# Kernel tuning notes

Hardware: AMD Instinct MI355X
Metric: run time of the kernel (lower is better)

The kernel has to match this reference:

```python
import jax, jax.numpy as jnp
import numpy as np

B, S, D, H, FF, L = 2, 2048, 512, 8, 2048, 2
HD = D // H
EPS = 1e-5
NEG = -1e9


def layernorm(x, gamma, beta):
    # mean/var over last axis (axis=2 in original)
    mean = jnp.mean(x, axis=-1, keepdims=True)
    var = jnp.mean((x - mean) ** 2, axis=-1, keepdims=True)
    return gamma * (x - mean) / jnp.sqrt(var + EPS) + beta


def masked_attention(x, mask, Wqkv, Wo, bo):
    b, s, d = x.shape
    qkv = x @ Wqkv                                  # [B,S,3D]
    qkv = qkv.reshape(b, s, H, 3 * HD)
    qkv = qkv.reshape(b, H, s, 3 * HD)              # original uses reshape, not transpose
    q, k, v = jnp.split(qkv, 3, axis=3)             # each [B,H,S,HD]
    scaled = jnp.einsum('bhqd,bhkd->bhqk', q, k) / (HD ** 0.5)
    col = mask[:, None, None, :]                    # valid key columns
    row = mask[:, None, :, None]                    # valid query rows
    logits = jnp.where(col, scaled, NEG)
    attn = jax.nn.softmax(logits, axis=-1)
    attn = attn * (row & col).astype(attn.dtype)    # exact zeros outside valid block
    values = jnp.einsum('bhqk,bhkd->bhqd', attn, v)  # [B,H,S,HD]
    values = values.reshape(b, s, H * HD)           # original uses reshape, not transpose
    return values @ Wo + bo


def encoder_layer(x, mask, p):
    res = x
    x = masked_attention(x, mask, p['Wqkv'], p['Wo'], p['bo'])
    x = layernorm(x + res, p['g1'], p['be1'])
    res = x
    x = jax.nn.relu(x @ p['W1'] + p['bf1']) @ p['W2'] + p['bf2']
    x = layernorm(x + res, p['g2'], p['be2'])
    return x


def setup_inputs() -> dict:
    key = jax.random.key(0)
    ks = jax.random.split(key, 8)
    x = jax.random.normal(ks[0], (B, S, D), jnp.float32)
    lengths = jax.random.randint(ks[1], (B,), S // 2, S + 1)
    paded_mask = jnp.arange(S)[None, :] < lengths[:, None]   # [B,S] bool
    sc = 0.02
    return {
        'x': x,
        'paded_mask': paded_mask,
        'Wqkv': jax.random.normal(ks[2], (L, D, 3 * D), jnp.float32) * sc,
        'Wo': jax.random.normal(ks[3], (L, D, D), jnp.float32) * sc,
        'bo': jnp.zeros((L, D), jnp.float32),
        'g1': jnp.ones((L, D), jnp.float32),
        'be1': jnp.zeros((L, D), jnp.float32),
        'W1': jax.random.normal(ks[4], (L, D, FF), jnp.float32) * sc,
        'bf1': jnp.zeros((L, FF), jnp.float32),
        'W2': jax.random.normal(ks[5], (L, FF, D), jnp.float32) * sc,
        'bf2': jnp.zeros((L, D), jnp.float32),
        'g2': jnp.ones((L, D), jnp.float32),
        'be2': jnp.zeros((L, D), jnp.float32),
    }


def reference(x, paded_mask, Wqkv, Wo, bo, g1, be1, W1, bf1, W2, bf2, g2, be2):
    for i in range(L):
        p = {'Wqkv': Wqkv[i], 'Wo': Wo[i], 'bo': bo[i], 'g1': g1[i], 'be1': be1[i],
             'W1': W1[i], 'bf1': bf1[i], 'W2': W2[i], 'bf2': bf2[i], 'g2': g2[i], 'be2': be2[i]}
        x = encoder_layer(x, paded_mask, p)
    return x
```

## Files before the change

### kernel.cpp

```cpp
#include <hip/hip_runtime.h>
#include <math.h>


typedef __bf16 bf16x8 __attribute__((ext_vector_type(8)));
typedef __bf16 bf16x4 __attribute__((ext_vector_type(4)));
typedef float f32x4 __attribute__((ext_vector_type(4)));

static constexpr int S_ = 2048;
static constexpr int D_ = 512;
static constexpr int FF_ = 2048;
static constexpr int M_ = 4096;

#define GLDS16(gp, lp)                                                      \
  __builtin_amdgcn_global_load_lds(                                         \
      (const __attribute__((address_space(1))) void*)(gp),                  \
      (__attribute__((address_space(3))) void*)(lp), 16, 0, 0)

__global__ __launch_bounds__(256) void prep_kernel(
    const float* __restrict__ Wqkv, const float* __restrict__ Wo,
    const float* __restrict__ W1, const float* __restrict__ W2,
    const float* __restrict__ x,
    __bf16* __restrict__ WqkvT, __bf16* __restrict__ WoT,
    __bf16* __restrict__ W1T, __bf16* __restrict__ W2T,
    __bf16* __restrict__ x_bf) {
  __shared__ float tile[32][33];
  const int t = threadIdx.x;
  int bid = blockIdx.x;
  if (bid >= 6144) {
    const size_t i = ((size_t)(bid - 6144) * 256 + t) * 8;
    float4 f0 = *(const float4*)(x + i), f1 = *(const float4*)(x + i + 4);
    bf16x8 v;
    v[0] = (__bf16)f0.x; v[1] = (__bf16)f0.y; v[2] = (__bf16)f0.z; v[3] = (__bf16)f0.w;
    v[4] = (__bf16)f1.x; v[5] = (__bf16)f1.y; v[6] = (__bf16)f1.z; v[7] = (__bf16)f1.w;
    *(bf16x8*)(x_bf + i) = v;
    return;
  }
  const float* W;
  __bf16* Wt;
  int K, N;
  if (bid < 1536)      { W = Wqkv;              Wt = WqkvT; K = 512;  N = 1536; }
  else if (bid < 2048) { bid -= 1536; W = Wo;   Wt = WoT;   K = 512;  N = 512; }
  else if (bid < 4096) { bid -= 2048; W = W1;   Wt = W1T;   K = 512;  N = 2048; }
  else                 { bid -= 4096; W = W2;   Wt = W2T;   K = 2048; N = 512; }
  const int nx = N >> 5, ny = K >> 5;
  const int xb = bid % nx, yb = (bid / nx) % ny, l = bid / (nx * ny);
  const size_t off = (size_t)l * K * N;
  const int n0 = xb * 32, k0 = yb * 32;
  const int tx = t & 31, ty = t >> 5;
#pragma unroll
  for (int i = 0; i < 4; ++i)
    tile[ty + i * 8][tx] = W[off + (size_t)(k0 + ty + i * 8) * N + n0 + tx];
  __syncthreads();
#pragma unroll
  for (int i = 0; i < 4; ++i)
    Wt[off + (size_t)(n0 + ty + i * 8) * K + k0 + tx] = (__bf16)tile[tx][ty + i * 8];
}

template <int BN, bool RELU, bool SPLITK2, bool QKV, bool OUT_BF16>
__global__ __launch_bounds__(256) void gemm_async(
    const __bf16* __restrict__ A, const __bf16* __restrict__ Wt,
    const float* __restrict__ bias, void* __restrict__ Cv,
    __bf16* __restrict__ VT, int M, int N, int K) {
  constexpr int BM = 128, BK = 64;
  constexpr int MI = 4;
  constexpr int NJ = BN / 32;
  __shared__ __bf16 As[BM][BK];
  __shared__ __bf16 Bs[BN][BK];

  const int t = threadIdx.x;
  const int wv = t >> 6, ln = t & 63;
  const int ln16 = t & 15, quad = (t & 63) >> 4;
  const int bm = blockIdx.x * BM, bn = blockIdx.y * BN;
  const int wm = (wv & 1) * 64, wn = (wv >> 1) * (BN / 2);

  int kbeg = 0, kend = K;
  if (SPLITK2) {
    const int half = K >> 1;
    kbeg = blockIdx.z * half;
    kend = kbeg + half;
  }

  f32x4 acc[MI][NJ];
#pragma unroll
  for (int i = 0; i < MI; ++i)
#pragma unroll
    for (int j = 0; j < NJ; ++j) acc[i][j] = {0.f, 0.f, 0.f, 0.f};

  for (int k0 = kbeg; k0 < kend; k0 += BK) {
#pragma unroll
    for (int it = 0; it < 4; ++it) {
      const int cb = it * 256 + wv * 64;
      const int c = cb + ln;
      const int r = c >> 3, jl = (c & 7) ^ (r & 7);
      GLDS16(A + (size_t)(bm + r) * K + k0 + jl * 8,
             (char*)&As[0][0] + (size_t)cb * 16);
    }
#pragma unroll
    for (int it = 0; it < BN / 32; ++it) {
      const int cb = it * 256 + wv * 64;
      const int c = cb + ln;
      const int r = c >> 3, jl = (c & 7) ^ (r & 7);
      GLDS16(Wt + (size_t)(bn + r) * K + k0 + jl * 8,
             (char*)&Bs[0][0] + (size_t)cb * 16);
    }
    __syncthreads();

#pragma unroll
    for (int kk = 0; kk < 2; ++kk) {
      bf16x8 a[MI], b[NJ];
#pragma unroll
      for (int i = 0; i < MI; ++i) {
        const int r = wm + i * 16 + ln16;
        a[i] = *(const bf16x8*)&As[r][((kk * 4 + quad) ^ (r & 7)) * 8];
      }
#pragma unroll
      for (int j = 0; j < NJ; ++j) {
        const int r = wn + j * 16 + ln16;
        b[j] = *(const bf16x8*)&Bs[r][((kk * 4 + quad) ^ (r & 7)) * 8];
      }
#pragma unroll
      for (int i = 0; i < MI; ++i)
#pragma unroll
        for (int j = 0; j < NJ; ++j)
          acc[i][j] = __builtin_amdgcn_mfma_f32_16x16x32_bf16(a[i], b[j], acc[i][j], 0, 0, 0);
    }
    __syncthreads();
  }

  float* Cs = (float*)Cv;
  if (SPLITK2) Cs += (size_t)blockIdx.z * M * N;
  const bool addb = bias && (!SPLITK2 || blockIdx.z == 0);
  const int bidx = bm >> 11;
#pragma unroll
  for (int i = 0; i < MI; ++i) {
#pragma unroll
    for (int j = 0; j < NJ; ++j) {
      const int col = bn + wn + j * 16 + ln16;
      if (QKV && (col % 192) >= 128) {
        const int d = col % 192 - 128;
        const int n8 = col / 192;
#pragma unroll
        for (int r = 0; r < 4; ++r) {
          const int s = (bm + wm + i * 16 + quad * 4 + r) & 2047;
          const int h = s >> 8;
          const int s2 = ((s & 255) << 3) | n8;
          VT[(((size_t)(bidx * 8 + h) * 64 + d) << 11) + s2] = (__bf16)acc[i][j][r];
        }
      } else {
        const float bv = addb ? bias[col] : 0.f;
#pragma unroll
        for (int r = 0; r < 4; ++r) {
          const int row = bm + wm + i * 16 + quad * 4 + r;
          float v = acc[i][j][r] + bv;
          if (RELU) v = fmaxf(v, 0.f);
          if (OUT_BF16)
            ((__bf16*)Cv)[(size_t)row * N + col] = (__bf16)v;
          else
            Cs[(size_t)row * N + col] = v;
        }
      }
    }
  }
}

__global__ __launch_bounds__(256) void attn_mfma(
    const __bf16* __restrict__ qkv, const __bf16* __restrict__ VT,
    const int* __restrict__ mask, __bf16* __restrict__ O) {
  const int b = blockIdx.z;
  const int h = blockIdx.y;
  const int q0 = blockIdx.x * 64;
  const int t = threadIdx.x;
  const int wq = t >> 6, ln16 = t & 15, quad = (t & 63) >> 4;

  __shared__ __bf16 Ks[64][72];
  __shared__ __bf16 Vt[64][72];
  __shared__ __bf16 Ps[64][72];
  __shared__ int lred[4];
  __shared__ int len_sh;

  const __bf16* base = qkv + (size_t)b * S_ * 1536 + (size_t)h * S_ * 192;
  const __bf16* vbase = VT + ((size_t)(b * 8 + h) << 17);
  __bf16* obase = O + (size_t)b * S_ * 512 + h * 64;

  {
    int c = 0;
    const int* mp = mask + b * S_ + t * 8;
#pragma unroll
    for (int i = 0; i < 8; ++i) c += mp[i];
#pragma unroll
    for (int off = 32; off >= 1; off >>= 1) c += __shfl_down(c, off, 64);
    if ((t & 63) == 0) lred[t >> 6] = c;
  }
  __syncthreads();
  if (t == 0) len_sh = lred[0] + lred[1] + lred[2] + lred[3];
  __syncthreads();
  const int len = len_sh;

  if (q0 >= len) {
    const int r = t >> 2, c16 = (t & 3) * 16;
    bf16x8 z = {};
    *(bf16x8*)(obase + (size_t)(q0 + r) * 512 + c16) = z;
    *(bf16x8*)(obase + (size_t)(q0 + r) * 512 + c16 + 8) = z;
    return;
  }

  bf16x8 aq[2];
  {
    const int q = q0 + wq * 16 + ln16;
    aq[0] = *(const bf16x8*)(base + (size_t)q * 192 + quad * 8);
    aq[1] = *(const bf16x8*)(base + (size_t)q * 192 + 32 + quad * 8);
  }

  float lpart = 0.f;
  f32x4 o[4];
#pragma unroll
  for (int d = 0; d < 4; ++d) o[d] = {0.f, 0.f, 0.f, 0.f};

  const int kr = t >> 3, kc = (t & 7) * 8;
  const int vd = t >> 2, vc = (t & 3) * 16;
  const int vphys = vc ^ ((vd & 3) * 16);

  bf16x8 kreg[2], vreg[2];
  auto fetch = [&](int kt) {
    kreg[0] = *(const bf16x8*)(base + (size_t)(kt + kr) * 192 + 64 + kc);
    kreg[1] = *(const bf16x8*)(base + (size_t)(kt + kr + 32) * 192 + 64 + kc);
    const __bf16* vp = vbase + (size_t)vd * 2048 + kt + vc;
    vreg[0] = *(const bf16x8*)vp;
    vreg[1] = *(const bf16x8*)(vp + 8);
  };

  fetch(0);

  for (int k0 = 0; k0 < len; k0 += 64) {
    *(bf16x8*)&Ks[kr][kc] = kreg[0];
    *(bf16x8*)&Ks[kr + 32][kc] = kreg[1];
    *(bf16x8*)&Vt[vd][vphys] = vreg[0];
    *(bf16x8*)&Vt[vd][vphys + 8] = vreg[1];
    __syncthreads();

    { const int kp = (k0 + 64 < S_) ? k0 + 64 : k0; fetch(kp); }

    f32x4 sf[4];
#pragma unroll
    for (int j = 0; j < 4; ++j) sf[j] = {0.f, 0.f, 0.f, 0.f};
#pragma unroll
    for (int kk = 0; kk < 2; ++kk) {
#pragma unroll
      for (int j = 0; j < 4; ++j) {
        bf16x8 ak = *(const bf16x8*)&Ks[j * 16 + ln16][kk * 32 + quad * 8];
        sf[j] = __builtin_amdgcn_mfma_f32_16x16x32_bf16(ak, aq[kk], sf[j], 0, 0, 0);
      }
    }

#pragma unroll
    for (int j = 0; j < 4; ++j) {
      bf16x4 pk;
#pragma unroll
      for (int r = 0; r < 4; ++r) {
        const float e = __expf(fminf(sf[j][r] * 0.125f, 60.f));
        const float p = (k0 + j * 16 + quad * 4 + r < len) ? e : 0.f;
        lpart += p;
        pk[r] = (__bf16)p;
      }
      *(bf16x4*)&Ps[wq * 16 + ln16][j * 16 + quad * 4] = pk;
    }
    asm volatile("s_waitcnt lgkmcnt(0)" ::: "memory");

#pragma unroll
    for (int kk = 0; kk < 2; ++kk) {
      bf16x8 pb = *(const bf16x8*)&Ps[wq * 16 + ln16][kk * 32 + quad * 8];
#pragma unroll
      for (int dt = 0; dt < 4; ++dt) {
        bf16x8 av = *(const bf16x8*)
            &Vt[dt * 16 + ln16][(kk * 32 + quad * 8) ^ ((ln16 & 3) * 16)];
        o[dt] = __builtin_amdgcn_mfma_f32_16x16x32_bf16(av, pb, o[dt], 0, 0, 0);
      }
    }
    __syncthreads();
  }

  lpart += __shfl_xor(lpart, 16, 64);
  lpart += __shfl_xor(lpart, 32, 64);

  const int q = q0 + wq * 16 + ln16;
  const float s = (q < len) ? 1.f / lpart : 0.f;
#pragma unroll
  for (int dt = 0; dt < 4; ++dt) {
    bf16x4 ov;
#pragma unroll
    for (int r = 0; r < 4; ++r) ov[r] = (__bf16)(o[dt][r] * s);
    *(bf16x4*)(obase + (size_t)q * 512 + dt * 16 + quad * 4) = ov;
  }
}

__global__ __launch_bounds__(256) void add_ln_kernel(
    const float* __restrict__ a, const float* __restrict__ a2,
    const float* __restrict__ res, const float* __restrict__ g,
    const float* __restrict__ be, float* __restrict__ out,
    __bf16* __restrict__ out_bf) {
  const int row = blockIdx.x * 4 + (threadIdx.x >> 6);
  const int ln = threadIdx.x & 63;
  const int c = ln * 8;
  const float* pa = a + (size_t)row * D_ + c;
  const float* pr = res + (size_t)row * D_ + c;

  float4 v0 = *(const float4*)pa, v1 = *(const float4*)(pa + 4);
  float4 r0 = *(const float4*)pr, r1 = *(const float4*)(pr + 4);
  float w[8] = {v0.x + r0.x, v0.y + r0.y, v0.z + r0.z, v0.w + r0.w,
                v1.x + r1.x, v1.y + r1.y, v1.z + r1.z, v1.w + r1.w};
  if (a2) {
    const float* p2 = a2 + (size_t)row * D_ + c;
    float4 u0 = *(const float4*)p2, u1 = *(const float4*)(p2 + 4);
    w[0] += u0.x; w[1] += u0.y; w[2] += u0.z; w[3] += u0.w;
    w[4] += u1.x; w[5] += u1.y; w[6] += u1.z; w[7] += u1.w;
  }
  float s = 0.f, sq = 0.f;
#pragma unroll
  for (int e = 0; e < 8; ++e) {
    s += w[e];
    sq += w[e] * w[e];
  }
#pragma unroll
  for (int off = 1; off < 64; off <<= 1) {
    s += __shfl_xor(s, off, 64);
    sq += __shfl_xor(sq, off, 64);
  }
  const float mean = s * (1.0f / D_);
  const float var = sq * (1.0f / D_) - mean * mean;
  const float rstd = rsqrtf(var + 1e-5f);

  float4 g0 = *(const float4*)(g + c), g1 = *(const float4*)(g + c + 4);
  float4 b0 = *(const float4*)(be + c), b1 = *(const float4*)(be + c + 4);
  const float gv[8] = {g0.x, g0.y, g0.z, g0.w, g1.x, g1.y, g1.z, g1.w};
  const float bv[8] = {b0.x, b0.y, b0.z, b0.w, b1.x, b1.y, b1.z, b1.w};
  float y[8];
#pragma unroll
  for (int e = 0; e < 8; ++e) y[e] = gv[e] * (w[e] - mean) * rstd + bv[e];

  float* po = out + (size_t)row * D_ + c;
  *(float4*)po = make_float4(y[0], y[1], y[2], y[3]);
  *(float4*)(po + 4) = make_float4(y[4], y[5], y[6], y[7]);
  if (out_bf) {
    bf16x8 v;
#pragma unroll
    for (int e = 0; e < 8; ++e) v[e] = (__bf16)y[e];
    *(bf16x8*)(out_bf + (size_t)row * D_ + c) = v;
  }
}

extern "C" void kernel_launch(void* const* d_in, const int* in_sizes, int n_in,
                              void* d_out, int out_size, void* d_ws, size_t ws_size,
                              hipStream_t stream) {
  const float* x_in = (const float*)d_in[0];
  const int* mask   = (const int*)d_in[1];
  const float* Wqkv = (const float*)d_in[2];
  const float* Wo   = (const float*)d_in[3];
  const float* bo   = (const float*)d_in[4];
  const float* g1   = (const float*)d_in[5];
  const float* be1  = (const float*)d_in[6];
  const float* W1   = (const float*)d_in[7];
  const float* bf1  = (const float*)d_in[8];
  const float* W2   = (const float*)d_in[9];
  const float* bf2  = (const float*)d_in[10];
  const float* g2   = (const float*)d_in[11];
  const float* be2  = (const float*)d_in[12];
  float* out = (float*)d_out;

  char* w = (char*)d_ws;
  auto alloc = [&](size_t bytes) {
    char* p = w;
    w += (bytes + 255) & ~(size_t)255;
    return p;
  };
  __bf16* WqkvT = (__bf16*)alloc((size_t)2 * 512 * 1536 * 2);
  __bf16* WoT   = (__bf16*)alloc((size_t)2 * 512 * 512 * 2);
  __bf16* W1T   = (__bf16*)alloc((size_t)2 * 512 * 2048 * 2);
  __bf16* W2T   = (__bf16*)alloc((size_t)2 * 2048 * 512 * 2);
  __bf16* R1    = (__bf16*)alloc((size_t)M_ * FF_ * 2);
  __bf16* VTb   = (__bf16*)alloc((size_t)16 * 64 * 2048 * 2);
  float* R2     = (float*)alloc((size_t)2 * M_ * D_ * 4);
  __bf16* Obf   = (__bf16*)alloc((size_t)M_ * D_ * 2);
  float* proj   = (float*)alloc((size_t)M_ * D_ * 4);
  float* x1     = (float*)alloc((size_t)M_ * D_ * 4);
  float* xE     = (float*)alloc((size_t)M_ * D_ * 4);
  __bf16* x_bf  = (__bf16*)alloc((size_t)M_ * D_ * 2);
  __bf16* x1_bf = (__bf16*)alloc((size_t)M_ * D_ * 2);
  __bf16* xE_bf = (__bf16*)alloc((size_t)M_ * D_ * 2);

  prep_kernel<<<dim3(7168), 256, 0, stream>>>(Wqkv, Wo, W1, W2, x_in,
                                              WqkvT, WoT, W1T, W2T, x_bf);

  for (int l = 0; l < 2; ++l) {
    const float* xin = (l == 0) ? x_in : xE;
    const __bf16* xin_bf = (l == 0) ? x_bf : xE_bf;
    float* xout = (l == 1) ? out : xE;
    __bf16* xout_bf = (l == 0) ? xE_bf : nullptr;
    const __bf16* WqkvT_l = WqkvT + (size_t)l * 512 * 1536;
    const __bf16* WoT_l   = WoT + (size_t)l * 512 * 512;
    const __bf16* W1T_l   = W1T + (size_t)l * 512 * 2048;
    const __bf16* W2T_l   = W2T + (size_t)l * 2048 * 512;

    gemm_async<64, false, false, true, true><<<dim3(32, 24), 256, 0, stream>>>(
        xin_bf, WqkvT_l, nullptr, R1, VTb, M_, 1536, 512);
    attn_mfma<<<dim3(S_ / 64, 8, 2), 256, 0, stream>>>(R1, VTb, mask, Obf);
    gemm_async<64, false, false, false, false><<<dim3(32, 8), 256, 0, stream>>>(
        Obf, WoT_l, bo + (size_t)l * D_, proj, nullptr, M_, 512, 512);
    add_ln_kernel<<<dim3(M_ / 4), 256, 0, stream>>>(proj, nullptr, xin,
                                                    g1 + (size_t)l * D_,
                                                    be1 + (size_t)l * D_, x1, x1_bf);
    gemm_async<128, true, false, false, true><<<dim3(32, 16), 256, 0, stream>>>(
        x1_bf, W1T_l, bf1 + (size_t)l * FF_, R1, nullptr, M_, 2048, 512);
    gemm_async<64, false, true, false, false><<<dim3(32, 8, 2), 256, 0, stream>>>(
        R1, W2T_l, bf2 + (size_t)l * D_, R2, nullptr, M_, 512, 2048);
    add_ln_kernel<<<dim3(M_ / 4), 256, 0, stream>>>(R2, R2 + (size_t)M_ * D_, x1,
                                                    g2 + (size_t)l * D_,
                                                    be2 + (size_t)l * D_, xout, xout_bf);
  }
}
```

Before: 351.7 us.

## Split attention key range across two thread groups per block and merge partials

```diff
diff --git a/kernel.cpp b/kernel.cpp
--- a/kernel.cpp
+++ b/kernel.cpp
@@ -163,18 +163,21 @@
   }
 }
 
-__global__ __launch_bounds__(256) void attn_mfma(
+__global__ __launch_bounds__(512) void attn_mfma(
     const __bf16* __restrict__ qkv, const __bf16* __restrict__ VT,
     const int* __restrict__ mask, __bf16* __restrict__ O) {
   const int b = blockIdx.z;
   const int h = blockIdx.y;
   const int q0 = blockIdx.x * 64;
   const int t = threadIdx.x;
-  const int wq = t >> 6, ln16 = t & 15, quad = (t & 63) >> 4;
-
-  __shared__ __bf16 Ks[64][72];
-  __shared__ __bf16 Vt[64][72];
-  __shared__ __bf16 Ps[64][72];
+  const int g = t >> 8;
+  const int tl = t & 255;
+  const int wq = tl >> 6;
+  const int ln16 = t & 15, quad = (t & 63) >> 4;
+
+  __shared__ __bf16 Ks[2][64][72];
+  __shared__ __bf16 Vt[2][64][72];
+  __shared__ __bf16 Ps[2][64][72];
   __shared__ int lred[4];
   __shared__ int len_sh;
 
@@ -182,7 +185,7 @@
   const __bf16* vbase = VT + ((size_t)(b * 8 + h) << 17);
   __bf16* obase = O + (size_t)b * S_ * 512 + h * 64;
 
-  {
+  if (t < 256) {
     int c = 0;
     const int* mp = mask + b * S_ + t * 8;
 #pragma unroll
@@ -197,10 +200,9 @@
   const int len = len_sh;
 
   if (q0 >= len) {
-    const int r = t >> 2, c16 = (t & 3) * 16;
+    const int r = t >> 3, c = (t & 7) * 8;
     bf16x8 z = {};
-    *(bf16x8*)(obase + (size_t)(q0 + r) * 512 + c16) = z;
-    *(bf16x8*)(obase + (size_t)(q0 + r) * 512 + c16 + 8) = z;
+    *(bf16x8*)(obase + (size_t)(q0 + r) * 512 + c) = z;
     return;
   }
 
@@ -216,8 +218,8 @@
 #pragma unroll
   for (int d = 0; d < 4; ++d) o[d] = {0.f, 0.f, 0.f, 0.f};
 
-  const int kr = t >> 3, kc = (t & 7) * 8;
-  const int vd = t >> 2, vc = (t & 3) * 16;
+  const int kr = tl >> 3, kc = (tl & 7) * 8;
+  const int vd = tl >> 2, vc = (tl & 3) * 16;
   const int vphys = vc ^ ((vd & 3) * 16);
 
   bf16x8 kreg[2], vreg[2];
@@ -229,16 +231,22 @@
     vreg[1] = *(const bf16x8*)(vp + 8);
   };
 
-  fetch(0);
-
-  for (int k0 = 0; k0 < len; k0 += 64) {
-    *(bf16x8*)&Ks[kr][kc] = kreg[0];
-    *(bf16x8*)&Ks[kr + 32][kc] = kreg[1];
-    *(bf16x8*)&Vt[vd][vphys] = vreg[0];
-    *(bf16x8*)&Vt[vd][vphys + 8] = vreg[1];
+  fetch(g * 64);
+
+  const int nit = (len + 127) >> 7;
+  for (int i = 0; i < nit; ++i) {
+    const int k0 = g * 64 + i * 128;
+    *(bf16x8*)&Ks[g][kr][kc] = kreg[0];
+    *(bf16x8*)&Ks[g][kr + 32][kc] = kreg[1];
+    *(bf16x8*)&Vt[g][vd][vphys] = vreg[0];
+    *(bf16x8*)&Vt[g][vd][vphys + 8] = vreg[1];
     __syncthreads();
 
-    { const int kp = (k0 + 64 < S_) ? k0 + 64 : k0; fetch(kp); }
+    {
+      int kp = k0 + 128;
+      if (kp > S_ - 64) kp = k0;
+      fetch(kp);
+    }
 
     f32x4 sf[4];
 #pragma unroll
@@ -247,7 +255,7 @@
     for (int kk = 0; kk < 2; ++kk) {
 #pragma unroll
       for (int j = 0; j < 4; ++j) {
-        bf16x8 ak = *(const bf16x8*)&Ks[j * 16 + ln16][kk * 32 + quad * 8];
+        bf16x8 ak = *(const bf16x8*)&Ks[g][j * 16 + ln16][kk * 32 + quad * 8];
         sf[j] = __builtin_amdgcn_mfma_f32_16x16x32_bf16(ak, aq[kk], sf[j], 0, 0, 0);
       }
     }
@@ -262,17 +270,17 @@
         lpart += p;
         pk[r] = (__bf16)p;
       }
-      *(bf16x4*)&Ps[wq * 16 + ln16][j * 16 + quad * 4] = pk;
+      *(bf16x4*)&Ps[g][wq * 16 + ln16][j * 16 + quad * 4] = pk;
     }
     asm volatile("s_waitcnt lgkmcnt(0)" ::: "memory");
 
 #pragma unroll
     for (int kk = 0; kk < 2; ++kk) {
-      bf16x8 pb = *(const bf16x8*)&Ps[wq * 16 + ln16][kk * 32 + quad * 8];
+      bf16x8 pb = *(const bf16x8*)&Ps[g][wq * 16 + ln16][kk * 32 + quad * 8];
 #pragma unroll
       for (int dt = 0; dt < 4; ++dt) {
         bf16x8 av = *(const bf16x8*)
-            &Vt[dt * 16 + ln16][(kk * 32 + quad * 8) ^ ((ln16 & 3) * 16)];
+            &Vt[g][dt * 16 + ln16][(kk * 32 + quad * 8) ^ ((ln16 & 3) * 16)];
         o[dt] = __builtin_amdgcn_mfma_f32_16x16x32_bf16(av, pb, o[dt], 0, 0, 0);
       }
     }
@@ -282,14 +290,28 @@
   lpart += __shfl_xor(lpart, 16, 64);
   lpart += __shfl_xor(lpart, 32, 64);
 
-  const int q = q0 + wq * 16 + ln16;
-  const float s = (q < len) ? 1.f / lpart : 0.f;
-#pragma unroll
-  for (int dt = 0; dt < 4; ++dt) {
-    bf16x4 ov;
-#pragma unroll
-    for (int r = 0; r < 4; ++r) ov[r] = (__bf16)(o[dt][r] * s);
-    *(bf16x4*)(obase + (size_t)q * 512 + dt * 16 + quad * 4) = ov;
+  float* obuf = (float*)&Ks[0][0][0];
+  float* lbuf = (float*)&Vt[0][0][0];
+  const int row = wq * 16 + ln16;
+  if (g == 1) {
+#pragma unroll
+    for (int dt = 0; dt < 4; ++dt)
+      *(f32x4*)&obuf[row * 64 + dt * 16 + quad * 4] = o[dt];
+    if (quad == 0) lbuf[row] = lpart;
+  }
+  __syncthreads();
+  if (g == 0) {
+    const int q = q0 + row;
+    const float l = lpart + lbuf[row];
+    const float s = (q < len) ? 1.f / l : 0.f;
+#pragma unroll
+    for (int dt = 0; dt < 4; ++dt) {
+      const f32x4 o1 = *(const f32x4*)&obuf[row * 64 + dt * 16 + quad * 4];
+      bf16x4 ov;
+#pragma unroll
+      for (int r = 0; r < 4; ++r) ov[r] = (__bf16)((o[dt][r] + o1[r]) * s);
+      *(bf16x4*)(obase + (size_t)q * 512 + dt * 16 + quad * 4) = ov;
+    }
   }
 }
 
@@ -402,7 +424,7 @@
 
     gemm_async<64, false, false, true, true><<<dim3(32, 24), 256, 0, stream>>>(
         xin_bf, WqkvT_l, nullptr, R1, VTb, M_, 1536, 512);
-    attn_mfma<<<dim3(S_ / 64, 8, 2), 256, 0, stream>>>(R1, VTb, mask, Obf);
+    attn_mfma<<<dim3(S_ / 64, 8, 2), 512, 0, stream>>>(R1, VTb, mask, Obf);
     gemm_async<64, false, false, false, false><<<dim3(32, 8), 256, 0, stream>>>(
         Obf, WoT_l, bo + (size_t)l * D_, proj, nullptr, M_, 512, 512);
     add_ln_kernel<<<dim3(M_ / 4), 256, 0, stream>>>(proj, nullptr, xin,
```

Result: faster. 340.0 us (-3.3%).

## Split attention key range across two blocks with atomic-ticket merge

Applied to the files above, without the earlier changes.

```diff
diff --git a/kernel.cpp b/kernel.cpp
--- a/kernel.cpp
+++ b/kernel.cpp
@@ -10,6 +10,7 @@
 static constexpr int D_ = 512;
 static constexpr int FF_ = 2048;
 static constexpr int M_ = 4096;
+static constexpr int PSLOT_ = 64 * 64 + 64;
 
 #define GLDS16(gp, lp)                                                      \
   __builtin_amdgcn_global_load_lds(                                         \
@@ -22,10 +23,14 @@
     const float* __restrict__ x,
     __bf16* __restrict__ WqkvT, __bf16* __restrict__ WoT,
     __bf16* __restrict__ W1T, __bf16* __restrict__ W2T,
-    __bf16* __restrict__ x_bf) {
+    __bf16* __restrict__ x_bf, int* __restrict__ flags) {
   __shared__ float tile[32][33];
   const int t = threadIdx.x;
   int bid = blockIdx.x;
+  if (bid == 0) {
+    int4 z; z.x = z.y = z.z = z.w = 0;
+    ((int4*)flags)[t] = z;
+  }
   if (bid >= 6144) {
     const size_t i = ((size_t)(bid - 6144) * 256 + t) * 8;
     float4 f0 = *(const float4*)(x + i), f1 = *(const float4*)(x + i + 4);
@@ -165,10 +170,12 @@
 
 __global__ __launch_bounds__(256) void attn_mfma(
     const __bf16* __restrict__ qkv, const __bf16* __restrict__ VT,
-    const int* __restrict__ mask, __bf16* __restrict__ O) {
-  const int b = blockIdx.z;
+    const int* __restrict__ mask, float* __restrict__ Apart,
+    int* __restrict__ flags, __bf16* __restrict__ O) {
+  const int b = blockIdx.z >> 1, chunk = blockIdx.z & 1;
   const int h = blockIdx.y;
-  const int q0 = blockIdx.x * 64;
+  const int qb = blockIdx.x;
+  const int q0 = qb * 64;
   const int t = threadIdx.x;
   const int wq = t >> 6, ln16 = t & 15, quad = (t & 63) >> 4;
 
@@ -177,6 +184,7 @@
   __shared__ __bf16 Ps[64][72];
   __shared__ int lred[4];
   __shared__ int len_sh;
+  __shared__ int tick_sh;
 
   const __bf16* base = qkv + (size_t)b * S_ * 1536 + (size_t)h * S_ * 192;
   const __bf16* vbase = VT + ((size_t)(b * 8 + h) << 17);
@@ -197,10 +205,12 @@
   const int len = len_sh;
 
   if (q0 >= len) {
-    const int r = t >> 2, c16 = (t & 3) * 16;
-    bf16x8 z = {};
-    *(bf16x8*)(obase + (size_t)(q0 + r) * 512 + c16) = z;
-    *(bf16x8*)(obase + (size_t)(q0 + r) * 512 + c16 + 8) = z;
+    if (chunk == 0) {
+      const int r = t >> 2, c = (t & 3) * 16;
+      bf16x8 z = {};
+      *(bf16x8*)(obase + (size_t)(q0 + r) * 512 + c) = z;
+      *(bf16x8*)(obase + (size_t)(q0 + r) * 512 + c + 8) = z;
+    }
     return;
   }
 
@@ -229,16 +239,20 @@
     vreg[1] = *(const bf16x8*)(vp + 8);
   };
 
-  fetch(0);
-
-  for (int k0 = 0; k0 < len; k0 += 64) {
+  fetch(chunk * 64);
+
+  for (int k0 = chunk * 64; k0 < len; k0 += 128) {
     *(bf16x8*)&Ks[kr][kc] = kreg[0];
     *(bf16x8*)&Ks[kr + 32][kc] = kreg[1];
     *(bf16x8*)&Vt[vd][vphys] = vreg[0];
     *(bf16x8*)&Vt[vd][vphys + 8] = vreg[1];
     __syncthreads();
 
-    { const int kp = (k0 + 64 < S_) ? k0 + 64 : k0; fetch(kp); }
+    {
+      int kp = k0 + 128;
+      if (kp > S_ - 64) kp = k0;
+      fetch(kp);
+    }
 
     f32x4 sf[4];
 #pragma unroll
@@ -252,17 +266,31 @@
       }
     }
 
-#pragma unroll
-    for (int j = 0; j < 4; ++j) {
-      bf16x4 pk;
-#pragma unroll
-      for (int r = 0; r < 4; ++r) {
-        const float e = __expf(fminf(sf[j][r] * 0.125f, 60.f));
-        const float p = (k0 + j * 16 + quad * 4 + r < len) ? e : 0.f;
-        lpart += p;
-        pk[r] = (__bf16)p;
-      }
-      *(bf16x4*)&Ps[wq * 16 + ln16][j * 16 + quad * 4] = pk;
+    if (k0 + 64 <= len) {
+#pragma unroll
+      for (int j = 0; j < 4; ++j) {
+        bf16x4 pk;
+#pragma unroll
+        for (int r = 0; r < 4; ++r) {
+          const float p = exp2f(fminf(sf[j][r] * 0.18033688f, 86.5617f));
+          lpart += p;
+          pk[r] = (__bf16)p;
+        }
+        *(bf16x4*)&Ps[wq * 16 + ln16][j * 16 + quad * 4] = pk;
+      }
+    } else {
+#pragma unroll
+      for (int j = 0; j < 4; ++j) {
+        bf16x4 pk;
+#pragma unroll
+        for (int r = 0; r < 4; ++r) {
+          const float e = exp2f(fminf(sf[j][r] * 0.18033688f, 86.5617f));
+          const float p = (k0 + j * 16 + quad * 4 + r < len) ? e : 0.f;
+          lpart += p;
+          pk[r] = (__bf16)p;
+        }
+        *(bf16x4*)&Ps[wq * 16 + ln16][j * 16 + quad * 4] = pk;
+      }
     }
     asm volatile("s_waitcnt lgkmcnt(0)" ::: "memory");
 
@@ -282,13 +310,32 @@
   lpart += __shfl_xor(lpart, 16, 64);
   lpart += __shfl_xor(lpart, 32, 64);
 
-  const int q = q0 + wq * 16 + ln16;
-  const float s = (q < len) ? 1.f / lpart : 0.f;
+  const int slot = (b * 8 + h) * 32 + qb;
+  const int row = wq * 16 + ln16;
+  {
+    float* my = Apart + ((size_t)chunk * 512 + slot) * PSLOT_;
+#pragma unroll
+    for (int dt = 0; dt < 4; ++dt)
+      *(f32x4*)(my + row * 64 + dt * 16 + quad * 4) = o[dt];
+    if (quad == 0) my[4096 + row] = lpart;
+  }
+  __syncthreads();
+  if (t == 0)
+    tick_sh = __hip_atomic_fetch_add(&flags[slot], 1, __ATOMIC_ACQ_REL,
+                                     __HIP_MEMORY_SCOPE_AGENT);
+  __syncthreads();
+  if (tick_sh == 0) return;
+
+  const float* ot = Apart + ((size_t)(1 - chunk) * 512 + slot) * PSLOT_;
+  const int q = q0 + row;
+  const float l = lpart + ot[4096 + row];
+  const float s = (q < len) ? 1.f / l : 0.f;
 #pragma unroll
   for (int dt = 0; dt < 4; ++dt) {
+    const f32x4 oo = *(const f32x4*)(ot + row * 64 + dt * 16 + quad * 4);
     bf16x4 ov;
 #pragma unroll
-    for (int r = 0; r < 4; ++r) ov[r] = (__bf16)(o[dt][r] * s);
+    for (int r = 0; r < 4; ++r) ov[r] = (__bf16)((o[dt][r] + oo[r]) * s);
     *(bf16x4*)(obase + (size_t)q * 512 + dt * 16 + quad * 4) = ov;
   }
 }
@@ -379,6 +426,8 @@
   __bf16* R1    = (__bf16*)alloc((size_t)M_ * FF_ * 2);
   __bf16* VTb   = (__bf16*)alloc((size_t)16 * 64 * 2048 * 2);
   float* R2     = (float*)alloc((size_t)2 * M_ * D_ * 4);
+  float* Apart  = (float*)alloc((size_t)2 * 512 * PSLOT_ * 4);
+  int*   flags  = (int*)alloc((size_t)1024 * 4);
   __bf16* Obf   = (__bf16*)alloc((size_t)M_ * D_ * 2);
   float* proj   = (float*)alloc((size_t)M_ * D_ * 4);
   float* x1     = (float*)alloc((size_t)M_ * D_ * 4);
@@ -388,7 +437,7 @@
   __bf16* xE_bf = (__bf16*)alloc((size_t)M_ * D_ * 2);
 
   prep_kernel<<<dim3(7168), 256, 0, stream>>>(Wqkv, Wo, W1, W2, x_in,
-                                              WqkvT, WoT, W1T, W2T, x_bf);
+                                              WqkvT, WoT, W1T, W2T, x_bf, flags);
 
   for (int l = 0; l < 2; ++l) {
     const float* xin = (l == 0) ? x_in : xE;
@@ -402,7 +451,8 @@
 
     gemm_async<64, false, false, true, true><<<dim3(32, 24), 256, 0, stream>>>(
         xin_bf, WqkvT_l, nullptr, R1, VTb, M_, 1536, 512);
-    attn_mfma<<<dim3(S_ / 64, 8, 2), 256, 0, stream>>>(R1, VTb, mask, Obf);
+    attn_mfma<<<dim3(S_ / 64, 8, 4), 256, 0, stream>>>(R1, VTb, mask, Apart,
+                                                       flags + l * 512, Obf);
     gemm_async<64, false, false, false, false><<<dim3(32, 8), 256, 0, stream>>>(
         Obf, WoT_l, bo + (size_t)l * D_, proj, nullptr, M_, 512, 512);
     add_ln_kernel<<<dim3(M_ / 4), 256, 0, stream>>>(proj, nullptr, xin,
```

New measurement: 404.2 us. 1.15x slower.
